# Performance work log

Measured on AMD Instinct MI355X. Metric: run time of the kernel, lower is better.

The kernel has to match this reference:

```python
import jax, jax.numpy as jnp
import numpy as np

IMG_SIZE = 608
NUM_CLASSES = 80
NUM_ANCHORS = 3
BBOX_ATTRS = 5 + NUM_CLASSES
ANCHORS = [
    [(10.0, 13.0), (16.0, 30.0), (33.0, 23.0)],    # stride 8  -> 76x76 grid
    [(30.0, 61.0), (62.0, 45.0), (59.0, 119.0)],   # stride 16 -> 38x38 grid
    [(116.0, 90.0), (156.0, 198.0), (373.0, 326.0)] # stride 32 -> 19x19 grid
]


def setup_inputs() -> dict:
    key = jax.random.key(0)
    k0, k1, k2 = jax.random.split(key, 3)
    bs = 16
    x0 = jax.random.normal(k0, (bs, NUM_ANCHORS * BBOX_ATTRS, 76, 76), dtype=jnp.float32)
    x1 = jax.random.normal(k1, (bs, NUM_ANCHORS * BBOX_ATTRS, 38, 38), dtype=jnp.float32)
    x2 = jax.random.normal(k2, (bs, NUM_ANCHORS * BBOX_ATTRS, 19, 19), dtype=jnp.float32)
    idf_logits = jnp.ones((NUM_CLASSES,), dtype=jnp.float32)
    return {"x0": x0, "x1": x1, "x2": x2, "idf_logits": idf_logits}


def _decode_scale(x, anchors, idf_logits):
    # x: [bs, A*attrs, H, W]
    bs, _, H, W = x.shape
    stride = IMG_SIZE / W  # square grid: stride_h == stride_w
    # view(bs, A, attrs, H, W).permute(0,3,4,1,2).reshape(bs, H*W*A, attrs)
    pred = x.reshape(bs, NUM_ANCHORS, BBOX_ATTRS, H, W)
    pred = jnp.transpose(pred, (0, 3, 4, 1, 2)).reshape(bs, H * W * NUM_ANCHORS, BBOX_ATTRS)
    # grid / anchor layout: ordering is (h, w, a) flattened, anchors fastest
    gx = (jnp.arange(W, dtype=jnp.float32) + 0.5)  # col index + 0.5
    gy = (jnp.arange(H, dtype=jnp.float32) + 0.5)  # row index + 0.5
    grid_x = jnp.broadcast_to(gx[None, :, None], (H, W, NUM_ANCHORS)).reshape(-1) / W
    grid_y = jnp.broadcast_to(gy[:, None, None], (H, W, NUM_ANCHORS)).reshape(-1) / H
    aw = jnp.asarray([a[0] / stride for a in anchors], dtype=jnp.float32) / W
    ah = jnp.asarray([a[1] / stride for a in anchors], dtype=jnp.float32) / H
    anchor_w = jnp.broadcast_to(aw[None, None, :], (H, W, NUM_ANCHORS)).reshape(-1)
    anchor_h = jnp.broadcast_to(ah[None, None, :], (H, W, NUM_ANCHORS)).reshape(-1)
    cxy = jnp.stack((grid_x, grid_y), axis=1)       # [HWA, 2]
    awh = jnp.stack((anchor_w, anchor_h), axis=1)   # [HWA, 2]
    in_w = jnp.float32(W)
    s = jnp.float32(stride)
    xy = (jax.nn.sigmoid(pred[..., 0:2]) + cxy[None] * in_w - 0.5) * s
    wh = jnp.exp(pred[..., 2:4]) * awh[None] * in_w * s
    conf = jax.nn.sigmoid(pred[..., 4:5])
    cls = jax.nn.sigmoid(idf_logits[None, None, :] * pred[..., 5:])
    return jnp.concatenate((xy, wh, conf, cls), axis=2)


def reference(x0, x1, x2, idf_logits):
    outs = [_decode_scale(x, anc, idf_logits)
            for x, anc in zip((x0, x1, x2), ANCHORS)]
    return jnp.concatenate(outs, axis=1)  # [bs, sum(H*W*A), 85]
```

## Files before the change

### kernel.cpp

```cpp
#include <hip/hip_runtime.h>
#include <cstddef>


#define NATTR 85
#define NCH 255
#define TILE 32
#define QPT 8
#define NSTG (NCH * QPT)

static constexpr int TOTROWS = (76 * 76 + 38 * 38 + 19 * 19) * 3;

static __device__ __forceinline__ float sigmoidf_(float x) {
  return 1.0f / (1.0f + __expf(-x));
}

template <int SCALE>
struct Cfg {
  static constexpr int W = (SCALE == 0) ? 76 : (SCALE == 1) ? 38 : 19;
  static constexpr int HW = W * W;
  static constexpr int TILES = (HW + TILE - 1) / TILE;
  static constexpr float STRIDE = 608.0f / (float)W;
  static constexpr int ROWBASE =
      (SCALE == 0) ? 0 : (SCALE == 1) ? 76 * 76 * 3 : (76 * 76 * 3 + 38 * 38 * 3);
  static constexpr float AW0 = (SCALE == 0) ? 10.f : (SCALE == 1) ? 30.f : 116.f;
  static constexpr float AW1 = (SCALE == 0) ? 16.f : (SCALE == 1) ? 62.f : 156.f;
  static constexpr float AW2 = (SCALE == 0) ? 33.f : (SCALE == 1) ? 59.f : 373.f;
  static constexpr float AH0 = (SCALE == 0) ? 13.f : (SCALE == 1) ? 61.f : 90.f;
  static constexpr float AH1 = (SCALE == 0) ? 30.f : (SCALE == 1) ? 45.f : 198.f;
  static constexpr float AH2 = (SCALE == 0) ? 23.f : (SCALE == 1) ? 119.f : 326.f;
};

template <int SCALE>
static __device__ __forceinline__ float xf(int a, int attr, int p, float v,
                                           const float* __restrict__ sidf) {
  using C = Cfg<SCALE>;
  if (attr >= 5) return sigmoidf_(sidf[attr - 5] * v);
  if (attr == 4) return sigmoidf_(v);
  if (attr == 2) {
    const float aw = (a == 0) ? C::AW0 : (a == 1) ? C::AW1 : C::AW2;
    return __expf(v) * aw;
  }
  if (attr == 3) {
    const float ah = (a == 0) ? C::AH0 : (a == 1) ? C::AH1 : C::AH2;
    return __expf(v) * ah;
  }
  const int h = p / C::W;
  const int w = p - h * C::W;
  return (sigmoidf_(v) + (float)((attr == 0) ? w : h)) * C::STRIDE;
}

template <int SCALE>
static __device__ __forceinline__ void decode_tile(
    int b, int t, const float* __restrict__ x, float* __restrict__ out,
    const float* __restrict__ sidf, float* __restrict__ lds) {
  using C = Cfg<SCALE>;
  const int p0 = t * TILE;
  const int rem = C::HW - p0;
  const int np = rem < TILE ? rem : TILE;
  const size_t off = ((size_t)b * TOTROWS + C::ROWBASE + (size_t)p0 * 3) * NATTR;
  const int head = (int)((4 - (off & 3)) & 3);
  const int s = (4 - head) & 3;
  const float* src = x + (size_t)b * ((size_t)C::HW * NCH) + p0;

  if ((C::HW % 4 == 0) && np == TILE) {
    float4 r[4];
    int cc[4], vv[4];
    bool act[4];
#pragma unroll
    for (int k = 0; k < 4; ++k) {
      int i = (int)threadIdx.x + 512 * k;
      act[k] = i < NSTG;
      i = act[k] ? i : (NSTG - 1);
      cc[k] = i >> 3;
      vv[k] = i & 7;
      r[k] = *reinterpret_cast<const float4*>(src + (size_t)cc[k] * C::HW + 4 * vv[k]);
    }
#pragma unroll
    for (int k = 0; k < 4; ++k) {
      if (act[k]) {
        const int c = cc[k];
        const int a = c / NATTR;
        const int attr = c - a * NATTR;
        const int pb = p0 + 4 * vv[k];
        float* dl = lds + s + (4 * vv[k]) * NCH + c;
        dl[0]       = xf<SCALE>(a, attr, pb + 0, r[k].x, sidf);
        dl[NCH]     = xf<SCALE>(a, attr, pb + 1, r[k].y, sidf);
        dl[2 * NCH] = xf<SCALE>(a, attr, pb + 2, r[k].z, sidf);
        dl[3 * NCH] = xf<SCALE>(a, attr, pb + 3, r[k].w, sidf);
      }
    }
  } else {
    for (int i = threadIdx.x; i < NCH * TILE; i += 512) {
      const int c = i >> 5;
      const int p = i & 31;
      if (p < np) {
        const int a = c / NATTR;
        const int attr = c - a * NATTR;
        const float v = src[(size_t)c * C::HW + p];
        lds[s + p * NCH + c] = xf<SCALE>(a, attr, p0 + p, v, sidf);
      }
    }
  }
  __syncthreads();

  float* dst = out + off;
  const int total = np * NCH;

  if (np == TILE) {
    if (threadIdx.x < head) dst[threadIdx.x] = lds[s + threadIdx.x];
    const int nvec = (total - head) >> 2;
    const float4* lv = reinterpret_cast<const float4*>(lds + s + head);
    float4 tt[4];
    int vi[4];
    bool av[4];
#pragma unroll
    for (int k = 0; k < 4; ++k) {
      int v = (int)threadIdx.x + 512 * k;
      av[k] = v < nvec;
      vi[k] = av[k] ? v : (nvec - 1);
      tt[k] = lv[vi[k]];
    }
#pragma unroll
    for (int k = 0; k < 4; ++k) {
      if (av[k]) *reinterpret_cast<float4*>(dst + head + 4 * vi[k]) = tt[k];
    }
    const int done = head + 4 * nvec;
    if (threadIdx.x < total - done) dst[done + threadIdx.x] = lds[s + done + threadIdx.x];
  } else {
    for (int j = threadIdx.x; j < total; j += 512) dst[j] = lds[s + j];
  }
}

__global__ __launch_bounds__(512, 8) void yolo_all(
    const float* __restrict__ x0, const float* __restrict__ x1,
    const float* __restrict__ x2, const float* __restrict__ idf,
    float* __restrict__ out, int bs) {
  __shared__ __align__(16) float lds[TILE * NCH + 4];
  __shared__ float sidf[80];
  if (threadIdx.x < 80) sidf[threadIdx.x] = idf[threadIdx.x];
  __syncthreads();

  const int nb0 = Cfg<0>::TILES * bs;
  const int nb1 = Cfg<1>::TILES * bs;
  int blk = blockIdx.x;
  if (blk < nb0) {
    decode_tile<0>(blk / Cfg<0>::TILES, blk % Cfg<0>::TILES, x0, out, sidf, lds);
  } else if (blk < nb0 + nb1) {
    blk -= nb0;
    decode_tile<1>(blk / Cfg<1>::TILES, blk % Cfg<1>::TILES, x1, out, sidf, lds);
  } else {
    blk -= nb0 + nb1;
    decode_tile<2>(blk / Cfg<2>::TILES, blk % Cfg<2>::TILES, x2, out, sidf, lds);
  }
}

extern "C" void kernel_launch(void* const* d_in, const int* in_sizes, int n_in,
                              void* d_out, int out_size, void* d_ws, size_t ws_size,
                              hipStream_t stream) {
  const float* x0 = (const float*)d_in[0];
  const float* x1 = (const float*)d_in[1];
  const float* x2 = (const float*)d_in[2];
  const float* idf = (const float*)d_in[3];
  float* out = (float*)d_out;

  const int bs = in_sizes[0] / (NCH * 76 * 76);
  const int nb = (Cfg<0>::TILES + Cfg<1>::TILES + Cfg<2>::TILES) * bs;

  yolo_all<<<dim3(nb), dim3(512), 0, stream>>>(x0, x1, x2, idf, out, bs);
}
```

Baseline: 55.06 us.

## Process two tiles per block with software-pipelined load/transform/store

Each block now handles two consecutive tiles. The global load of the second tile is issued while the first tile is read back from LDS, and the first tile's stores are issued before the second tile is transformed. This is meant to overlap global memory latency with LDS traffic, and it halves the grid size. `__syncthreads` is replaced by a custom barrier that waits only on LDS counters (`lgkmcnt`), so outstanding global loads stay in flight across it. The cost is more register pressure, and the launch code assumes every per-scale tile count is even, so an odd batch size would break.

Result: slower. 63.23 us (+14.8%).

```diff
diff --git a/kernel.cpp b/kernel.cpp
--- a/kernel.cpp
+++ b/kernel.cpp
@@ -7,11 +7,18 @@
 #define TILE 32
 #define QPT 8
 #define NSTG (NCH * QPT)
+#define NTHR 512
 
 static constexpr int TOTROWS = (76 * 76 + 38 * 38 + 19 * 19) * 3;
 
 static __device__ __forceinline__ float sigmoidf_(float x) {
   return 1.0f / (1.0f + __expf(-x));
+}
+
+static __device__ __forceinline__ void bar_lgkm() {
+  asm volatile("s_waitcnt lgkmcnt(0)" ::: "memory");
+  __builtin_amdgcn_s_barrier();
+  asm volatile("" ::: "memory");
 }
 
 template <int SCALE>
@@ -49,40 +56,64 @@
   return (sigmoidf_(v) + (float)((attr == 0) ? w : h)) * C::STRIDE;
 }
 
-template <int SCALE>
-static __device__ __forceinline__ void decode_tile(
-    int b, int t, const float* __restrict__ x, float* __restrict__ out,
-    const float* __restrict__ sidf, float* __restrict__ lds) {
-  using C = Cfg<SCALE>;
-  const int p0 = t * TILE;
-  const int rem = C::HW - p0;
-  const int np = rem < TILE ? rem : TILE;
-  const size_t off = ((size_t)b * TOTROWS + C::ROWBASE + (size_t)p0 * 3) * NATTR;
-  const int head = (int)((4 - (off & 3)) & 3);
-  const int s = (4 - head) & 3;
-  const float* src = x + (size_t)b * ((size_t)C::HW * NCH) + p0;
-
-  if ((C::HW % 4 == 0) && np == TILE) {
-    float4 r[4];
-    int cc[4], vv[4];
-    bool act[4];
-#pragma unroll
-    for (int k = 0; k < 4; ++k) {
-      int i = (int)threadIdx.x + 512 * k;
-      act[k] = i < NSTG;
-      i = act[k] ? i : (NSTG - 1);
-      cc[k] = i >> 3;
-      vv[k] = i & 7;
-      r[k] = *reinterpret_cast<const float4*>(src + (size_t)cc[k] * C::HW + 4 * vv[k]);
-    }
-#pragma unroll
-    for (int k = 0; k < 4; ++k) {
-      if (act[k]) {
-        const int c = cc[k];
+struct TState {
+  const float* src;
+  size_t off;
+  int p0, np, head, s;
+};
+
+template <int SCALE>
+static __device__ __forceinline__ void tile_init(int idx, const float* __restrict__ x,
+                                                 TState& st) {
+  using C = Cfg<SCALE>;
+  const int b = idx / C::TILES;
+  const int t = idx - b * C::TILES;
+  st.p0 = t * TILE;
+  const int rem = C::HW - st.p0;
+  st.np = rem < TILE ? rem : TILE;
+  st.off = ((size_t)b * TOTROWS + C::ROWBASE + (size_t)st.p0 * 3) * NATTR;
+  st.head = (int)((4 - (st.off & 3)) & 3);
+  st.s = (4 - st.head) & 3;
+  st.src = x + (size_t)b * ((size_t)C::HW * NCH) + st.p0;
+}
+
+template <int SCALE>
+static __device__ __forceinline__ void tile_load(const TState& st, float4 (&r)[4]) {
+  using C = Cfg<SCALE>;
+  if ((C::HW % 4 == 0) && st.np == TILE) {
+#pragma unroll
+    for (int k = 0; k < 4; ++k) {
+      int i = (int)threadIdx.x + NTHR * k;
+      i = i < NSTG ? i : NSTG - 1;
+      const int c = i >> 3, v = i & 7;
+      r[k] = *reinterpret_cast<const float4*>(st.src + (size_t)c * C::HW + 4 * v);
+    }
+  } else {
+    float* rf = reinterpret_cast<float*>(r);
+#pragma unroll
+    for (int k = 0; k < 16; ++k) {
+      const int i = (int)threadIdx.x + NTHR * k;
+      const int c = i >> 5, p = i & 31;
+      if (c < NCH && p < st.np) rf[k] = st.src[(size_t)c * C::HW + p];
+    }
+  }
+}
+
+template <int SCALE>
+static __device__ __forceinline__ void tile_xform(const TState& st, float4 (&r)[4],
+                                                  const float* __restrict__ sidf,
+                                                  float* __restrict__ lds) {
+  using C = Cfg<SCALE>;
+  if ((C::HW % 4 == 0) && st.np == TILE) {
+#pragma unroll
+    for (int k = 0; k < 4; ++k) {
+      const int i = (int)threadIdx.x + NTHR * k;
+      if (i < NSTG) {
+        const int c = i >> 3, v = i & 7;
         const int a = c / NATTR;
         const int attr = c - a * NATTR;
-        const int pb = p0 + 4 * vv[k];
-        float* dl = lds + s + (4 * vv[k]) * NCH + c;
+        const int pb = st.p0 + 4 * v;
+        float* dl = lds + st.s + (4 * v) * NCH + c;
         dl[0]       = xf<SCALE>(a, attr, pb + 0, r[k].x, sidf);
         dl[NCH]     = xf<SCALE>(a, attr, pb + 1, r[k].y, sidf);
         dl[2 * NCH] = xf<SCALE>(a, attr, pb + 2, r[k].z, sidf);
@@ -90,45 +121,93 @@
       }
     }
   } else {
-    for (int i = threadIdx.x; i < NCH * TILE; i += 512) {
-      const int c = i >> 5;
-      const int p = i & 31;
-      if (p < np) {
+    const float* rf = reinterpret_cast<const float*>(r);
+#pragma unroll
+    for (int k = 0; k < 16; ++k) {
+      const int i = (int)threadIdx.x + NTHR * k;
+      const int c = i >> 5, p = i & 31;
+      if (c < NCH && p < st.np) {
         const int a = c / NATTR;
         const int attr = c - a * NATTR;
-        const float v = src[(size_t)c * C::HW + p];
-        lds[s + p * NCH + c] = xf<SCALE>(a, attr, p0 + p, v, sidf);
+        lds[st.s + p * NCH + c] = xf<SCALE>(a, attr, st.p0 + p, rf[k], sidf);
       }
     }
   }
-  __syncthreads();
-
-  float* dst = out + off;
-  const int total = np * NCH;
-
-  if (np == TILE) {
-    if (threadIdx.x < head) dst[threadIdx.x] = lds[s + threadIdx.x];
-    const int nvec = (total - head) >> 2;
-    const float4* lv = reinterpret_cast<const float4*>(lds + s + head);
-    float4 tt[4];
-    int vi[4];
-    bool av[4];
-#pragma unroll
-    for (int k = 0; k < 4; ++k) {
-      int v = (int)threadIdx.x + 512 * k;
-      av[k] = v < nvec;
-      vi[k] = av[k] ? v : (nvec - 1);
-      tt[k] = lv[vi[k]];
-    }
-#pragma unroll
-    for (int k = 0; k < 4; ++k) {
-      if (av[k]) *reinterpret_cast<float4*>(dst + head + 4 * vi[k]) = tt[k];
-    }
-    const int done = head + 4 * nvec;
-    if (threadIdx.x < total - done) dst[done + threadIdx.x] = lds[s + done + threadIdx.x];
-  } else {
-    for (int j = threadIdx.x; j < total; j += 512) dst[j] = lds[s + j];
-  }
+}
+
+static __device__ __forceinline__ void tile_read(const TState& st,
+                                                 const float* __restrict__ lds,
+                                                 float4 (&tt)[4], float& hv, float& tv) {
+  const int total = st.np * NCH;
+  if ((st.np & 3) == 0) {
+    const int nvec = (total - st.head) >> 2;
+    const float4* lv = reinterpret_cast<const float4*>(lds + st.s + st.head);
+    if ((int)threadIdx.x < st.head) hv = lds[st.s + threadIdx.x];
+#pragma unroll
+    for (int k = 0; k < 4; ++k) {
+      int v = (int)threadIdx.x + NTHR * k;
+      v = v < nvec ? v : nvec - 1;
+      tt[k] = lv[v];
+    }
+    const int done = st.head + 4 * nvec;
+    if ((int)threadIdx.x < total - done) tv = lds[st.s + done + threadIdx.x];
+  } else {
+    float* tf = reinterpret_cast<float*>(tt);
+#pragma unroll
+    for (int m = 0; m < 5; ++m) {
+      const int j = (int)threadIdx.x + NTHR * m;
+      if (j < total) tf[m] = lds[st.s + j];
+    }
+  }
+}
+
+static __device__ __forceinline__ void tile_store(const TState& st, float4 (&tt)[4],
+                                                  float hv, float tv,
+                                                  float* __restrict__ out) {
+  const int total = st.np * NCH;
+  float* dst = out + st.off;
+  if ((st.np & 3) == 0) {
+    const int nvec = (total - st.head) >> 2;
+    if ((int)threadIdx.x < st.head) dst[threadIdx.x] = hv;
+#pragma unroll
+    for (int k = 0; k < 4; ++k) {
+      const int v = (int)threadIdx.x + NTHR * k;
+      if (v < nvec) *reinterpret_cast<float4*>(dst + st.head + 4 * v) = tt[k];
+    }
+    const int done = st.head + 4 * nvec;
+    if ((int)threadIdx.x < total - done) dst[done + threadIdx.x] = tv;
+  } else {
+    const float* tf = reinterpret_cast<const float*>(tt);
+#pragma unroll
+    for (int m = 0; m < 5; ++m) {
+      const int j = (int)threadIdx.x + NTHR * m;
+      if (j < total) dst[j] = tf[m];
+    }
+  }
+}
+
+template <int SCALE>
+static __device__ __forceinline__ void pipeline2(int i0, const float* __restrict__ x,
+                                                 const float* __restrict__ sidf,
+                                                 float* __restrict__ out,
+                                                 float* __restrict__ lds) {
+  TState s0, s1;
+  tile_init<SCALE>(i0, x, s0);
+  tile_init<SCALE>(i0 + 1, x, s1);
+  float4 r[4], tt[4];
+  float hv = 0.f, tv = 0.f;
+
+  tile_load<SCALE>(s0, r);
+  tile_xform<SCALE>(s0, r, sidf, lds);
+  bar_lgkm();
+  tile_read(s0, lds, tt, hv, tv);
+  tile_load<SCALE>(s1, r);
+  bar_lgkm();
+  tile_store(s0, tt, hv, tv, out);
+  tile_xform<SCALE>(s1, r, sidf, lds);
+  bar_lgkm();
+  tile_read(s1, lds, tt, hv, tv);
+  tile_store(s1, tt, hv, tv, out);
 }
 
 __global__ __launch_bounds__(512, 8) void yolo_all(
@@ -142,15 +221,13 @@
 
   const int nb0 = Cfg<0>::TILES * bs;
   const int nb1 = Cfg<1>::TILES * bs;
-  int blk = blockIdx.x;
-  if (blk < nb0) {
-    decode_tile<0>(blk / Cfg<0>::TILES, blk % Cfg<0>::TILES, x0, out, sidf, lds);
-  } else if (blk < nb0 + nb1) {
-    blk -= nb0;
-    decode_tile<1>(blk / Cfg<1>::TILES, blk % Cfg<1>::TILES, x1, out, sidf, lds);
-  } else {
-    blk -= nb0 + nb1;
-    decode_tile<2>(blk / Cfg<2>::TILES, blk % Cfg<2>::TILES, x2, out, sidf, lds);
+  const int g0 = blockIdx.x * 2;
+  if (g0 < nb0) {
+    pipeline2<0>(g0, x0, sidf, out, lds);
+  } else if (g0 < nb0 + nb1) {
+    pipeline2<1>(g0 - nb0, x1, sidf, out, lds);
+  } else {
+    pipeline2<2>(g0 - nb0 - nb1, x2, sidf, out, lds);
   }
 }
 
@@ -164,7 +241,8 @@
   float* out = (float*)d_out;
 
   const int bs = in_sizes[0] / (NCH * 76 * 76);
-  const int nb = (Cfg<0>::TILES + Cfg<1>::TILES + Cfg<2>::TILES) * bs;
+  const int ntiles = (Cfg<0>::TILES + Cfg<1>::TILES + Cfg<2>::TILES) * bs;
+  const int nb = ntiles / 2;
 
   yolo_all<<<dim3(nb), dim3(512), 0, stream>>>(x0, x1, x2, idf, out, bs);
 }
```
